# Kernel optimization log

Hardware: AMD Instinct MI355X
Metric: run time of the kernel (lower is better)

Reference implementation:

```python
import jax, jax.numpy as jnp
import numpy as np

TEMPERATURE = 0.5
EPS = 1e-8  # torch CosineSimilarity eps
NEG_INF = -1e9


def setup_inputs() -> dict:
    key = jax.random.key(0)
    k1, k2 = jax.random.split(key)
    B, D = 4096, 256
    return {
        "z_i": jax.random.normal(k1, (B, D), dtype=jnp.float32),
        "z_j": jax.random.normal(k2, (B, D), dtype=jnp.float32),
    }


def reference(z_i, z_j):
    B = z_i.shape[0]
    N = 2 * B
    z = jnp.concatenate([z_i, z_j], axis=0)  # [N, D]
    # Cosine similarity = GEMM of L2-normalized rows (same math as broadcasted CosineSimilarity)
    zn = z / jnp.maximum(jnp.linalg.norm(z, axis=1, keepdims=True), EPS)
    sim = (zn @ zn.T) / TEMPERATURE  # [N, N]
    # Positives: the (i, i+B) and (i+B, i) off-diagonals
    pos = jnp.concatenate([jnp.diagonal(sim, B), jnp.diagonal(sim, -B)])  # [N]
    # CE with label 0 over logits = [positive, negatives...]. The logit set per row
    # equals the sim row minus its self-diagonal entry (positive appears exactly once).
    sim_masked = jnp.where(jnp.eye(N, dtype=bool), NEG_INF, sim)
    lse = jax.nn.logsumexp(sim_masked, axis=1)  # [N]
    # CrossEntropyLoss(reduction='sum') / N == mean over rows
    return jnp.mean(lse - pos)
```

## Files before the change

kernel.cpp:

```cpp
#include <hip/hip_runtime.h>
#include <hip/hip_bf16.h>

#define NN 8192
#define DD 256
#define BB 4096
#define CSPLIT 16
#define COLS_PER_SPLIT (NN / CSPLIT)
#define COLTILE 64
#define TEMP_SCALE 2.0f

typedef __attribute__((ext_vector_type(8))) short short8;
typedef __attribute__((ext_vector_type(4))) float f32x4;

static __device__ inline ushort f2bf(float x) {
    __hip_bfloat16 h = __float2bfloat16(x);
    return *reinterpret_cast<ushort*>(&h);
}

__global__ __launch_bounds__(256) void norm_kernel(const float* __restrict__ zi,
                                                   const float* __restrict__ zj,
                                                   ushort* __restrict__ zn) {
    int row  = (blockIdx.x * 256 + threadIdx.x) >> 6;
    int lane = threadIdx.x & 63;
    if (row >= NN) return;
    const float* src = (row < BB) ? (zi + (size_t)row * DD)
                                  : (zj + (size_t)(row - BB) * DD);
    float4 v = ((const float4*)src)[lane];
    float ss = v.x * v.x + v.y * v.y + v.z * v.z + v.w * v.w;
    #pragma unroll
    for (int m = 32; m; m >>= 1) ss += __shfl_xor(ss, m, 64);
    float inv = 1.0f / fmaxf(sqrtf(ss), 1e-8f);
    ushort4 o;
    o.x = f2bf(v.x * inv);
    o.y = f2bf(v.y * inv);
    o.z = f2bf(v.z * inv);
    o.w = f2bf(v.w * inv);
    ((ushort4*)(zn + (size_t)row * DD))[lane] = o;
}

__global__ __launch_bounds__(256, 2) void sim_kernel(const ushort* __restrict__ zn,
                                                     float* __restrict__ psum,
                                                     float* __restrict__ pos) {
    __shared__ int4 lds4[COLTILE * 32];

    const int tid  = threadIdx.x;
    const int wid  = tid >> 6;
    const int lane = tid & 63;
    const int l15  = lane & 15;
    const int lhi  = lane >> 4;

    const int row0     = blockIdx.x * 256 + wid * 64;
    const int colbase0 = blockIdx.y * COLS_PER_SPLIT;

    short8 a[4][8];
    #pragma unroll
    for (int rt = 0; rt < 4; ++rt)
        #pragma unroll
        for (int kk = 0; kk < 8; ++kk) {
            const ushort* p = zn + (size_t)(row0 + rt * 16 + l15) * DD + kk * 32 + lhi * 8;
            a[rt][kk] = *(const short8*)p;
        }

    f32x4 sume[4];
    #pragma unroll
    for (int rt = 0; rt < 4; ++rt) sume[rt] = (f32x4){0.f, 0.f, 0.f, 0.f};

    for (int ct = 0; ct < COLS_PER_SPLIT; ct += COLTILE) {
        const int colb = colbase0 + ct;
        __syncthreads();
        #pragma unroll
        for (int i = 0; i < 8; ++i) {
            int g   = tid + i * 256;
            int r   = g >> 5;
            int c16 = g & 31;
            int4 v = *(const int4*)(zn + (size_t)(colb + r) * DD + c16 * 8);
            lds4[r * 32 + (c16 ^ (r & 7))] = v;
        }
        __syncthreads();

        #pragma unroll
        for (int sub = 0; sub < 4; ++sub) {
            const int brow = sub * 16 + l15;
            short8 b[8];
            #pragma unroll
            for (int kk = 0; kk < 8; ++kk) {
                int gidx = brow * 32 + ((kk * 4 + lhi) ^ (brow & 7));
                b[kk] = ((const short8*)lds4)[gidx];
            }
            const int gc = colb + brow;
            #pragma unroll
            for (int rt = 0; rt < 4; ++rt) {
                f32x4 acc = (f32x4){0.f, 0.f, 0.f, 0.f};
                #pragma unroll
                for (int kk = 0; kk < 8; ++kk)
                    acc = __builtin_amdgcn_mfma_f32_16x16x32_bf16(a[rt][kk], b[kk], acc, 0, 0, 0);
                #pragma unroll
                for (int reg = 0; reg < 4; ++reg) {
                    int gr  = row0 + rt * 16 + lhi * 4 + reg;
                    float s = acc[reg] * TEMP_SCALE;
                    float e = (gc == gr) ? 0.0f : __expf(s);
                    sume[rt][reg] += e;
                    if (gc == (gr ^ BB)) pos[gr] = s;
                }
            }
        }
    }

    #pragma unroll
    for (int rt = 0; rt < 4; ++rt) {
        #pragma unroll
        for (int reg = 0; reg < 4; ++reg) {
            float v = sume[rt][reg];
            v += __shfl_xor(v, 1, 64);
            v += __shfl_xor(v, 2, 64);
            v += __shfl_xor(v, 4, 64);
            v += __shfl_xor(v, 8, 64);
            if (l15 == 0) {
                int gr = row0 + rt * 16 + lhi * 4 + reg;
                psum[(size_t)blockIdx.y * NN + gr] = v;
            }
        }
    }
}

__global__ __launch_bounds__(256) void reduce1(const float* __restrict__ psum,
                                               const float* __restrict__ pos,
                                               float* __restrict__ partial) {
    int r    = blockIdx.x * 256 + threadIdx.x;
    int lane = threadIdx.x & 63;
    int wid  = threadIdx.x >> 6;
    float sum = 0.f;
    #pragma unroll
    for (int s = 0; s < CSPLIT; ++s) sum += psum[(size_t)s * NN + r];
    float v = logf(sum) - pos[r];
    #pragma unroll
    for (int m = 32; m; m >>= 1) v += __shfl_xor(v, m, 64);
    __shared__ float red[4];
    if (lane == 0) red[wid] = v;
    __syncthreads();
    if (threadIdx.x == 0) partial[blockIdx.x] = red[0] + red[1] + red[2] + red[3];
}

__global__ void reduce2(const float* __restrict__ partial, float* __restrict__ out) {
    int lane = threadIdx.x & 63;
    float v = (lane < 32) ? partial[lane] : 0.f;
    #pragma unroll
    for (int m = 32; m; m >>= 1) v += __shfl_xor(v, m, 64);
    if (lane == 0) out[0] = v * (1.0f / NN);
}

extern "C" void kernel_launch(void* const* d_in, const int* in_sizes, int n_in,
                              void* d_out, int out_size, void* d_ws, size_t ws_size,
                              hipStream_t stream) {
    const float* zi = (const float*)d_in[0];
    const float* zj = (const float*)d_in[1];
    float* out = (float*)d_out;

    char* ws = (char*)d_ws;
    ushort* zn     = (ushort*)ws;
    size_t  off    = (size_t)NN * DD * 2;
    float*  psum   = (float*)(ws + off);  off += (size_t)CSPLIT * NN * 4;
    float*  pos    = (float*)(ws + off);  off += (size_t)NN * 4;
    float*  partial= (float*)(ws + off);

    norm_kernel<<<NN / 4, 256, 0, stream>>>(zi, zj, zn);
    dim3 g2(NN / 256, CSPLIT);
    sim_kernel<<<g2, 256, 0, stream>>>(zn, psum, pos);
    reduce1<<<NN / 256, 256, 0, stream>>>(psum, pos, partial);
    reduce2<<<1, 64, 0, stream>>>(partial, out);
}
```

Baseline: 125.2 us.

## Exploit symmetry of similarity matrix with triangular tiles and exp2 prescaling

Computes only upper-triangular 128x128 tiles of the symmetric similarity matrix and adds each tile's exp-sums to both the row and column accumulators through atomics. Folds the temperature and log2(e) into a second pre-scaled bf16 copy of the normalized rows so the exponent becomes a raw exp2 instruction. Removes the diagonal masking and positive extraction from the hot loop and recomputes both as dot products in the final reduction, which now atomically accumulates the loss. Also double-buffers the column tiles with direct global-to-LDS loads. In exchange it adds atomics and a diagonal subtraction that is sensitive to bf16 rounding.

```diff
diff --git a/kernel.cpp b/kernel.cpp
--- a/kernel.cpp
+++ b/kernel.cpp
@@ -2,27 +2,43 @@
 #include <hip/hip_bf16.h>
 
 #define NN 8192
+#define BB 4096
 #define DD 256
-#define BB 4096
-#define CSPLIT 16
-#define COLS_PER_SPLIT (NN / CSPLIT)
-#define COLTILE 64
-#define TEMP_SCALE 2.0f
+#define TILE 128
+#define NT (NN / TILE)
+#define NBLK (NT * (NT + 1) / 2)
+#define KSCALE 2.8853900817779268f
 
 typedef __attribute__((ext_vector_type(8))) short short8;
 typedef __attribute__((ext_vector_type(4))) float f32x4;
 
-static __device__ inline ushort f2bf(float x) {
+#if defined(__has_builtin)
+#if __has_builtin(__builtin_amdgcn_exp2f)
+#define EXP2F(x) __builtin_amdgcn_exp2f(x)
+#endif
+#endif
+#ifndef EXP2F
+static __device__ __forceinline__ float exp2_asm(float x) {
+    float r; asm("v_exp_f32 %0, %1" : "=v"(r) : "v"(x)); return r;
+}
+#define EXP2F(x) exp2_asm(x)
+#endif
+
+static __device__ __forceinline__ ushort f2bf(float x) {
     __hip_bfloat16 h = __float2bfloat16(x);
     return *reinterpret_cast<ushort*>(&h);
 }
+static __device__ __forceinline__ float bf2f(short u) {
+    unsigned int x = (unsigned int)(ushort)u << 16;
+    float f; __builtin_memcpy(&f, &x, 4); return f;
+}
 
 __global__ __launch_bounds__(256) void norm_kernel(const float* __restrict__ zi,
                                                    const float* __restrict__ zj,
-                                                   ushort* __restrict__ zn) {
+                                                   ushort* __restrict__ zn,
+                                                   ushort* __restrict__ zns) {
     int row  = (blockIdx.x * 256 + threadIdx.x) >> 6;
     int lane = threadIdx.x & 63;
-    if (row >= NN) return;
     const float* src = (row < BB) ? (zi + (size_t)row * DD)
                                   : (zj + (size_t)(row - BB) * DD);
     float4 v = ((const float4*)src)[lane];
@@ -30,123 +46,140 @@
     #pragma unroll
     for (int m = 32; m; m >>= 1) ss += __shfl_xor(ss, m, 64);
     float inv = 1.0f / fmaxf(sqrtf(ss), 1e-8f);
-    ushort4 o;
-    o.x = f2bf(v.x * inv);
-    o.y = f2bf(v.y * inv);
-    o.z = f2bf(v.z * inv);
-    o.w = f2bf(v.w * inv);
-    ((ushort4*)(zn + (size_t)row * DD))[lane] = o;
-}
-
-__global__ __launch_bounds__(256, 2) void sim_kernel(const ushort* __restrict__ zn,
-                                                     float* __restrict__ psum,
-                                                     float* __restrict__ pos) {
-    __shared__ int4 lds4[COLTILE * 32];
+    ushort4 o, os;
+    o.x  = f2bf(v.x * inv);            o.y  = f2bf(v.y * inv);
+    o.z  = f2bf(v.z * inv);            o.w  = f2bf(v.w * inv);
+    float invs = inv * KSCALE;
+    os.x = f2bf(v.x * invs);           os.y = f2bf(v.y * invs);
+    os.z = f2bf(v.z * invs);           os.w = f2bf(v.w * invs);
+    ((ushort4*)(zn  + (size_t)row * DD))[lane] = o;
+    ((ushort4*)(zns + (size_t)row * DD))[lane] = os;
+}
+
+__global__ __launch_bounds__(256, 4) void sim_kernel(const ushort* __restrict__ zn,
+                                                     const ushort* __restrict__ zns,
+                                                     float* __restrict__ psum) {
+    __shared__ int4  lds4[2][1024];
+    __shared__ float csum[TILE];
 
     const int tid  = threadIdx.x;
-    const int wid  = tid >> 6;
+    const int w    = tid >> 6;
     const int lane = tid & 63;
     const int l15  = lane & 15;
     const int lhi  = lane >> 4;
 
-    const int row0     = blockIdx.x * 256 + wid * 64;
-    const int colbase0 = blockIdx.y * COLS_PER_SPLIT;
-
-    short8 a[4][8];
-    #pragma unroll
-    for (int rt = 0; rt < 4; ++rt)
+    int idx = blockIdx.x;
+    int bj  = (int)((sqrtf(8.0f * (float)idx + 1.0f) - 1.0f) * 0.5f);
+    while ((bj + 1) * (bj + 2) / 2 <= idx) ++bj;
+    while (bj * (bj + 1) / 2 > idx) --bj;
+    int bi = idx - bj * (bj + 1) / 2;
+
+    const int  rowbase = bi * TILE + w * 32;
+    const int  colbase = bj * TILE;
+    const bool offdiag = (bi != bj);
+
+    if (tid < TILE) csum[tid] = 0.f;
+
+    short8 a0[8], a1[8];
+    #pragma unroll
+    for (int kk = 0; kk < 8; ++kk) {
+        a0[kk] = *(const short8*)(zns + (size_t)(rowbase + l15)      * DD + kk * 32 + lhi * 8);
+        a1[kk] = *(const short8*)(zns + (size_t)(rowbase + 16 + l15) * DD + kk * 32 + lhi * 8);
+    }
+
+    f32x4 sume0 = {0.f, 0.f, 0.f, 0.f}, sume1 = {0.f, 0.f, 0.f, 0.f};
+
+    auto STAGE = [&](int buf, int ct) {
+        const ushort* base = zn + (size_t)(colbase + ct * 32) * DD;
         #pragma unroll
-        for (int kk = 0; kk < 8; ++kk) {
-            const ushort* p = zn + (size_t)(row0 + rt * 16 + l15) * DD + kk * 32 + lhi * 8;
-            a[rt][kk] = *(const short8*)p;
+        for (int i = 0; i < 4; ++i) {
+            int d = w * 256 + i * 64 + lane;
+            int r = d >> 5, c = d & 31;
+            const ushort* src = base + (size_t)r * DD + (size_t)((c ^ (r & 7)) * 8);
+            __builtin_amdgcn_global_load_lds(
+                (__attribute__((address_space(1))) void*)src,
+                (__attribute__((address_space(3))) void*)&lds4[buf][w * 256 + i * 64],
+                16, 0, 0);
         }
-
-    f32x4 sume[4];
-    #pragma unroll
-    for (int rt = 0; rt < 4; ++rt) sume[rt] = (f32x4){0.f, 0.f, 0.f, 0.f};
-
-    for (int ct = 0; ct < COLS_PER_SPLIT; ct += COLTILE) {
-        const int colb = colbase0 + ct;
-        __syncthreads();
+    };
+
+    STAGE(0, 0);
+    __syncthreads();
+
+    for (int ct = 0; ct < 4; ++ct) {
+        if (ct < 3) STAGE((ct + 1) & 1, ct + 1);
+        const short8* buf = (const short8*)lds4[ct & 1];
         #pragma unroll
-        for (int i = 0; i < 8; ++i) {
-            int g   = tid + i * 256;
-            int r   = g >> 5;
-            int c16 = g & 31;
-            int4 v = *(const int4*)(zn + (size_t)(colb + r) * DD + c16 * 8);
-            lds4[r * 32 + (c16 ^ (r & 7))] = v;
+        for (int sub = 0; sub < 2; ++sub) {
+            const int brow = sub * 16 + l15;
+            f32x4 acc0 = {0.f, 0.f, 0.f, 0.f}, acc1 = {0.f, 0.f, 0.f, 0.f};
+            #pragma unroll
+            for (int kk = 0; kk < 8; ++kk) {
+                short8 b = buf[brow * 32 + ((kk * 4 + lhi) ^ (brow & 7))];
+                acc0 = __builtin_amdgcn_mfma_f32_16x16x32_bf16(a0[kk], b, acc0, 0, 0, 0);
+                acc1 = __builtin_amdgcn_mfma_f32_16x16x32_bf16(a1[kk], b, acc1, 0, 0, 0);
+            }
+            float cs = 0.f;
+            #pragma unroll
+            for (int g = 0; g < 4; ++g) {
+                float e0 = EXP2F(acc0[g]);
+                float e1 = EXP2F(acc1[g]);
+                sume0[g] += e0;
+                sume1[g] += e1;
+                cs += e0 + e1;
+            }
+            if (offdiag) {
+                cs += __shfl_xor(cs, 16, 64);
+                cs += __shfl_xor(cs, 32, 64);
+                if (lhi == 0) atomicAdd(&csum[ct * 32 + sub * 16 + l15], cs);
+            }
         }
         __syncthreads();
-
-        #pragma unroll
-        for (int sub = 0; sub < 4; ++sub) {
-            const int brow = sub * 16 + l15;
-            short8 b[8];
-            #pragma unroll
-            for (int kk = 0; kk < 8; ++kk) {
-                int gidx = brow * 32 + ((kk * 4 + lhi) ^ (brow & 7));
-                b[kk] = ((const short8*)lds4)[gidx];
-            }
-            const int gc = colb + brow;
-            #pragma unroll
-            for (int rt = 0; rt < 4; ++rt) {
-                f32x4 acc = (f32x4){0.f, 0.f, 0.f, 0.f};
-                #pragma unroll
-                for (int kk = 0; kk < 8; ++kk)
-                    acc = __builtin_amdgcn_mfma_f32_16x16x32_bf16(a[rt][kk], b[kk], acc, 0, 0, 0);
-                #pragma unroll
-                for (int reg = 0; reg < 4; ++reg) {
-                    int gr  = row0 + rt * 16 + lhi * 4 + reg;
-                    float s = acc[reg] * TEMP_SCALE;
-                    float e = (gc == gr) ? 0.0f : __expf(s);
-                    sume[rt][reg] += e;
-                    if (gc == (gr ^ BB)) pos[gr] = s;
-                }
-            }
+    }
+
+    #pragma unroll
+    for (int g = 0; g < 4; ++g) {
+        float v0 = sume0[g], v1 = sume1[g];
+        v0 += __shfl_xor(v0, 1, 64); v0 += __shfl_xor(v0, 2, 64);
+        v0 += __shfl_xor(v0, 4, 64); v0 += __shfl_xor(v0, 8, 64);
+        v1 += __shfl_xor(v1, 1, 64); v1 += __shfl_xor(v1, 2, 64);
+        v1 += __shfl_xor(v1, 4, 64); v1 += __shfl_xor(v1, 8, 64);
+        if (l15 == 0) {
+            atomicAdd(&psum[rowbase + lhi * 4 + g],      v0);
+            atomicAdd(&psum[rowbase + 16 + lhi * 4 + g], v1);
         }
     }
-
-    #pragma unroll
-    for (int rt = 0; rt < 4; ++rt) {
-        #pragma unroll
-        for (int reg = 0; reg < 4; ++reg) {
-            float v = sume[rt][reg];
-            v += __shfl_xor(v, 1, 64);
-            v += __shfl_xor(v, 2, 64);
-            v += __shfl_xor(v, 4, 64);
-            v += __shfl_xor(v, 8, 64);
-            if (l15 == 0) {
-                int gr = row0 + rt * 16 + lhi * 4 + reg;
-                psum[(size_t)blockIdx.y * NN + gr] = v;
-            }
-        }
-    }
-}
-
-__global__ __launch_bounds__(256) void reduce1(const float* __restrict__ psum,
-                                               const float* __restrict__ pos,
-                                               float* __restrict__ partial) {
-    int r    = blockIdx.x * 256 + threadIdx.x;
-    int lane = threadIdx.x & 63;
-    int wid  = threadIdx.x >> 6;
-    float sum = 0.f;
-    #pragma unroll
-    for (int s = 0; s < CSPLIT; ++s) sum += psum[(size_t)s * NN + r];
-    float v = logf(sum) - pos[r];
-    #pragma unroll
-    for (int m = 32; m; m >>= 1) v += __shfl_xor(v, m, 64);
-    __shared__ float red[4];
-    if (lane == 0) red[wid] = v;
-    __syncthreads();
-    if (threadIdx.x == 0) partial[blockIdx.x] = red[0] + red[1] + red[2] + red[3];
-}
-
-__global__ void reduce2(const float* __restrict__ partial, float* __restrict__ out) {
-    int lane = threadIdx.x & 63;
-    float v = (lane < 32) ? partial[lane] : 0.f;
-    #pragma unroll
-    for (int m = 32; m; m >>= 1) v += __shfl_xor(v, m, 64);
-    if (lane == 0) out[0] = v * (1.0f / NN);
+    if (offdiag && tid < TILE) atomicAdd(&psum[colbase + tid], csum[tid]);
+}
+
+__global__ __launch_bounds__(256) void reduce1(const ushort* __restrict__ zn,
+                                               const ushort* __restrict__ zns,
+                                               const float* __restrict__ psum,
+                                               float* __restrict__ out) {
+    int r = blockIdx.x * 16 + (threadIdx.x >> 4);
+    int l = threadIdx.x & 15;
+    const ushort* zr = zn  + (size_t)r * DD + l * 16;
+    const ushort* sr = zns + (size_t)r * DD + l * 16;
+    const ushort* pr = zn  + (size_t)(r ^ BB) * DD + l * 16;
+    short8 z0 = *(const short8*)zr, z1 = *(const short8*)(zr + 8);
+    short8 s0 = *(const short8*)sr, s1 = *(const short8*)(sr + 8);
+    short8 p0 = *(const short8*)pr, p1 = *(const short8*)(pr + 8);
+    float ds = 0.f, dp = 0.f;
+    #pragma unroll
+    for (int k = 0; k < 8; ++k) {
+        float za = bf2f(z0[k]), zb = bf2f(z1[k]);
+        ds += bf2f(s0[k]) * za + bf2f(s1[k]) * zb;
+        dp += bf2f(p0[k]) * za + bf2f(p1[k]) * zb;
+    }
+    #pragma unroll
+    for (int m = 8; m; m >>= 1) {
+        ds += __shfl_xor(ds, m, 64);
+        dp += __shfl_xor(dp, m, 64);
+    }
+    if (l == 0) {
+        float val = logf(psum[r] - EXP2F(ds)) - 2.0f * dp;
+        atomicAdd(out, val * (1.0f / NN));
+    }
 }
 
 extern "C" void kernel_launch(void* const* d_in, const int* in_sizes, int n_in,
@@ -157,15 +190,13 @@
     float* out = (float*)d_out;
 
     char* ws = (char*)d_ws;
-    ushort* zn     = (ushort*)ws;
-    size_t  off    = (size_t)NN * DD * 2;
-    float*  psum   = (float*)(ws + off);  off += (size_t)CSPLIT * NN * 4;
-    float*  pos    = (float*)(ws + off);  off += (size_t)NN * 4;
-    float*  partial= (float*)(ws + off);
-
-    norm_kernel<<<NN / 4, 256, 0, stream>>>(zi, zj, zn);
-    dim3 g2(NN / 256, CSPLIT);
-    sim_kernel<<<g2, 256, 0, stream>>>(zn, psum, pos);
-    reduce1<<<NN / 256, 256, 0, stream>>>(psum, pos, partial);
-    reduce2<<<1, 64, 0, stream>>>(partial, out);
-}
+    ushort* zn   = (ushort*)ws;
+    ushort* zns  = (ushort*)(ws + (size_t)NN * DD * 2);
+    float*  psum = (float*)(ws + (size_t)NN * DD * 4);
+
+    hipMemsetAsync(psum, 0, (size_t)NN * 4, stream);
+    hipMemsetAsync(out, 0, sizeof(float), stream);
+    norm_kernel<<<NN / 4, 256, 0, stream>>>(zi, zj, zn, zns);
+    sim_kernel<<<NBLK, 256, 0, stream>>>(zn, zns, psum);
+    reduce1<<<NN / 16, 256, 0, stream>>>(zn, zns, psum, out);
+}
```

New measurement: 138.5 us. +10.6%, slower.
